# Optimization experiments

Hardware: AMD Instinct MI355X
Metric: run time of the kernel (lower is better)

The kernel has to match this reference:

```python
import jax, jax.numpy as jnp
import numpy as np

N_EMB = 1024
N_HEAD = 16
HEAD_SIZE = N_EMB // N_HEAD  # 64
B, T = 4, 4096


def setup_inputs() -> dict:
    key = jax.random.key(0)
    kx, kq, kk, kv = jax.random.split(key, 4)
    x = jax.random.normal(kx, (B, T, N_EMB), dtype=jnp.float32)
    # torch nn.Linear(in=N_EMB, out=HEAD_SIZE, bias=False) weight: [out, in]
    s = 1.0 / np.sqrt(N_EMB)
    Wq = jax.random.uniform(kq, (HEAD_SIZE, N_EMB), jnp.float32, -s, s)
    Wk = jax.random.uniform(kk, (HEAD_SIZE, N_EMB), jnp.float32, -s, s)
    Wv = jax.random.uniform(kv, (HEAD_SIZE, N_EMB), jnp.float32, -s, s)
    return {"x": x, "Wq": Wq, "Wk": Wk, "Wv": Wv}


def reference(x, Wq, Wk, Wv):
    # q,k,v: [B,T,H]
    q = jnp.einsum('btc,hc->bth', x, Wq)
    k = jnp.einsum('btc,hc->bth', x, Wk)
    v = jnp.einsum('btc,hc->bth', x, Wv)
    scale = HEAD_SIZE ** (-0.5)
    att = jnp.einsum('bth,bsh->bts', q, k) * scale  # [B,T,T]
    Tn = x.shape[1]
    causal = jnp.tril(jnp.ones((Tn, Tn), dtype=bool))
    att = jnp.where(causal, att, -jnp.inf)
    att = jax.nn.softmax(att, axis=-1)
    # dropout p=0.0 -> identity
    out = jnp.einsum('bts,bsh->bth', att, v)  # [B,T,H]
    return out
```

## Files before the change

### kernel.cpp

```cpp
#include <hip/hip_runtime.h>


typedef __attribute__((ext_vector_type(8))) short v8s;
typedef __attribute__((ext_vector_type(4))) float v4f;

static __device__ __forceinline__ unsigned short f2bf(float x) {
  unsigned int u = __builtin_bit_cast(unsigned int, x);
  u += 0x7fffu + ((u >> 16) & 1u);
  return (unsigned short)(u >> 16);
}

__global__ __launch_bounds__(256) void pack_w(const float* __restrict__ Wq,
                                              const float* __restrict__ Wk,
                                              const float* __restrict__ Wv,
                                              unsigned short* __restrict__ WF) {
  int idx = (blockIdx.x * 256 + threadIdx.x) * 4;
  int row = idx >> 10;
  int k   = idx & 1023;
  const float* src;
  float scale;
  if (row < 64)       { src = Wq + row * 1024 + k;         scale = 0.125f; }
  else if (row < 128) { src = Wk + (row - 64) * 1024 + k;  scale = 1.0f;   }
  else                { src = Wv + (row - 128) * 1024 + k; scale = 1.0f;   }
  float4 f = *(const float4*)src;
  ushort4 o;
  o.x = f2bf(f.x * scale); o.y = f2bf(f.y * scale);
  o.z = f2bf(f.z * scale); o.w = f2bf(f.w * scale);
  size_t off = ((size_t)((k >> 8) * 8 + ((k >> 5) & 7)) * 12 + (row >> 4)) * 512 +
               (((k >> 3) & 3) * 16 + (row & 15)) * 8 + (k & 7);
  *(ushort4*)(WF + off) = o;
}

__global__ __launch_bounds__(256, 2) void qkv(const float* __restrict__ x,
                                              const unsigned short* __restrict__ WF,
                                              unsigned short* __restrict__ Qg,
                                              unsigned short* __restrict__ KF,
                                              unsigned short* __restrict__ VF) {
  __shared__ float red[3][64][49];
  const int tid   = threadIdx.x;
  const int lane  = tid & 63;
  const int wv    = tid >> 6;
  const int quad  = lane >> 4;
  const int colid = lane & 15;
  const int row0  = blockIdx.x * 32;

  const float* xbase = x + (size_t)(row0 + colid) * 1024 + wv * 256 + quad * 8;
  const unsigned short* wfbase = WF + (size_t)wv * 8 * 12 * 512 + lane * 8;

  v4f acc[24];
#pragma unroll
  for (int i = 0; i < 24; i++) acc[i] = (v4f){0.f, 0.f, 0.f, 0.f};

#pragma unroll
  for (int step = 0; step < 8; step++) {
    v8s am[2];
#pragma unroll
    for (int mg = 0; mg < 2; mg++) {
      float4 f0 = *(const float4*)(xbase + (size_t)mg * 16 * 1024 + step * 32);
      float4 f1 = *(const float4*)(xbase + (size_t)mg * 16 * 1024 + step * 32 + 4);
      am[mg][0] = (short)f2bf(f0.x); am[mg][1] = (short)f2bf(f0.y);
      am[mg][2] = (short)f2bf(f0.z); am[mg][3] = (short)f2bf(f0.w);
      am[mg][4] = (short)f2bf(f1.x); am[mg][5] = (short)f2bf(f1.y);
      am[mg][6] = (short)f2bf(f1.z); am[mg][7] = (short)f2bf(f1.w);
    }
    v8s bt[12];
#pragma unroll
    for (int nt = 0; nt < 12; nt++)
      bt[nt] = *(const v8s*)(wfbase + (size_t)(step * 12 + nt) * 512);
#pragma unroll
    for (int nt = 0; nt < 12; nt++)
#pragma unroll
      for (int mg = 0; mg < 2; mg++)
        acc[mg * 12 + nt] =
            __builtin_amdgcn_mfma_f32_16x16x32_bf16(am[mg], bt[nt], acc[mg * 12 + nt], 0, 0, 0);
  }

#pragma unroll
  for (int mg = 0; mg < 2; mg++) {
    if (wv != 0) {
#pragma unroll
      for (int nt = 0; nt < 12; nt++)
#pragma unroll
        for (int r = 0; r < 4; r++)
          red[wv - 1][lane][nt * 4 + r] = acc[mg * 12 + nt][r];
    }
    __syncthreads();
    if (wv == 0) {
      const int trow_base = row0 + mg * 16 + quad * 4;
#pragma unroll
      for (int nt = 0; nt < 12; nt++) {
        float sum[4];
#pragma unroll
        for (int r = 0; r < 4; r++)
          sum[r] = acc[mg * 12 + nt][r] + red[0][lane][nt * 4 + r] +
                   red[1][lane][nt * 4 + r] + red[2][lane][nt * 4 + r];
        if (nt < 4) {
#pragma unroll
          for (int r = 0; r < 4; r++)
            Qg[(size_t)(trow_base + r) * 64 + nt * 16 + colid] = f2bf(sum[r]);
        } else if (nt < 8) {
          int half = (nt - 4) >> 1;
          int q_f  = ((nt - 4) * 2 + (colid >> 3)) & 3;
          int j    = colid & 7;
#pragma unroll
          for (int r = 0; r < 4; r++) {
            int t  = trow_base + r;
            int b  = t >> 12, tl = t & 4095;
            int si = tl >> 6, sl = tl & 63;
            KF[((size_t)(b * 64 + si) * 8 + (sl >> 4) * 2 + half) * 512 +
               (q_f * 16 + (sl & 15)) * 8 + j] = f2bf(sum[r]);
          }
        } else {
#pragma unroll
          for (int r = 0; r < 4; r++) {
            int t  = trow_base + r;
            int b  = t >> 12, tl = t & 4095;
            int si = tl >> 6;
            int half = (tl >> 5) & 1, q_f = (tl >> 3) & 3, j = tl & 7;
            VF[((size_t)(b * 64 + si) * 8 + (nt - 8) * 2 + half) * 512 +
               (q_f * 16 + colid) * 8 + j] = f2bf(sum[r]);
          }
        }
      }
    }
    __syncthreads();
  }
}

__global__ __launch_bounds__(256, 2) void flash(const unsigned short* __restrict__ Qg,
                                                const unsigned short* __restrict__ KF,
                                                const unsigned short* __restrict__ VF,
                                                float* __restrict__ out) {
  __shared__ alignas(16) char smem[4 * 32 * 68 * 4 + 4 * 32 * 4];
  unsigned short* pl = (unsigned short*)smem;
  float* redf = (float*)smem;
  float* lred = (float*)(smem + 4 * 32 * 68 * 4);

  const int tid   = threadIdx.x;
  const int lane  = tid & 63;
  const int wv    = tid >> 6;
  const int quad  = lane >> 4;
  const int colid = lane & 15;
  const int qt32  = 127 - (int)(blockIdx.x >> 2);
  const int b     = blockIdx.x & 3;
  const int bT    = b * 4096;
  const int row00 = qt32 * 32;
  const int qimax = (row00 + 31) >> 6;

  v8s qf[2][2];
#pragma unroll
  for (int mt = 0; mt < 2; mt++) {
    const unsigned short* qrow =
        Qg + (size_t)(bT + row00 + mt * 16 + colid) * 64 + quad * 8;
    qf[mt][0] = *(const v8s*)(qrow);
    qf[mt][1] = *(const v8s*)(qrow + 32);
  }

  v8s ones;
#pragma unroll
  for (int j = 0; j < 8; j++) ones[j] = (short)0x3F80;

  v4f o[2][4];
#pragma unroll
  for (int mt = 0; mt < 2; mt++)
#pragma unroll
    for (int i = 0; i < 4; i++) o[mt][i] = (v4f){0.f, 0.f, 0.f, 0.f};
  v4f lac[2];
  lac[0] = (v4f){0.f, 0.f, 0.f, 0.f};
  lac[1] = (v4f){0.f, 0.f, 0.f, 0.f};

  const unsigned short* kb0 = KF + (size_t)b * 64 * 4096 + lane * 8;
  const unsigned short* vb0 = VF + (size_t)b * 64 * 4096 + lane * 8;

  for (int si = wv; si <= qimax; si += 4) {
    const unsigned short* ktile = kb0 + (size_t)si * 4096;
    const unsigned short* vtile = vb0 + (size_t)si * 4096;
    v8s kbr[8], vfr[8];
#pragma unroll
    for (int c = 0; c < 8; c++) kbr[c] = *(const v8s*)(ktile + (size_t)c * 512);
#pragma unroll
    for (int c = 0; c < 8; c++) vfr[c] = *(const v8s*)(vtile + (size_t)c * 512);

#pragma unroll
    for (int mt = 0; mt < 2; mt++) {
      v4f s[4];
#pragma unroll
      for (int i = 0; i < 4; i++) s[i] = (v4f){0.f, 0.f, 0.f, 0.f};
#pragma unroll
      for (int nt = 0; nt < 4; nt++) {
        s[nt] = __builtin_amdgcn_mfma_f32_16x16x32_bf16(qf[mt][0], kbr[2 * nt], s[nt], 0, 0, 0);
        s[nt] = __builtin_amdgcn_mfma_f32_16x16x32_bf16(qf[mt][1], kbr[2 * nt + 1], s[nt], 0, 0, 0);
      }

      if (si == qimax) {
        int rowb = row00 + mt * 16 + quad * 4;
        int colb = si * 64;
#pragma unroll
        for (int nt = 0; nt < 4; nt++)
#pragma unroll
          for (int r = 0; r < 4; r++)
            if (colb + nt * 16 + colid > rowb + r) s[nt][r] = -1e30f;
      }

      unsigned short* pw = pl + (wv * 2 + mt) * (16 * 72);
#pragma unroll
      for (int nt = 0; nt < 4; nt++)
#pragma unroll
        for (int r = 0; r < 4; r++)
          pw[(quad * 4 + r) * 72 + nt * 16 + colid] = f2bf(__expf(s[nt][r]));
    }

#pragma unroll
    for (int mt = 0; mt < 2; mt++) {
      unsigned short* pw = pl + (wv * 2 + mt) * (16 * 72);
#pragma unroll
      for (int ks = 0; ks < 64; ks += 32) {
        v8s af = *(const v8s*)(&pw[colid * 72 + ks + quad * 8]);
        lac[mt] = __builtin_amdgcn_mfma_f32_16x16x32_bf16(af, ones, lac[mt], 0, 0, 0);
#pragma unroll
        for (int nt = 0; nt < 4; nt++)
          o[mt][nt] = __builtin_amdgcn_mfma_f32_16x16x32_bf16(
              af, vfr[2 * nt + (ks >> 5)], o[mt][nt], 0, 0, 0);
      }
    }
  }

  __syncthreads();
#pragma unroll
  for (int mt = 0; mt < 2; mt++) {
#pragma unroll
    for (int nt = 0; nt < 4; nt++)
#pragma unroll
      for (int r = 0; r < 4; r++)
        redf[(wv * 32 + mt * 16 + quad * 4 + r) * 68 + nt * 16 + colid] = o[mt][nt][r];
    if (colid == 0) {
#pragma unroll
      for (int r = 0; r < 4; r++)
        lred[wv * 32 + mt * 16 + quad * 4 + r] = lac[mt][r];
    }
  }
  __syncthreads();

  {
    int col = tid & 63;
    int r0  = tid >> 6;
#pragma unroll
    for (int rr = 0; rr < 8; rr++) {
      int row = r0 * 8 + rr;
      float sum = 0.f, lsum = 0.f;
#pragma unroll
      for (int w = 0; w < 4; w++) {
        sum  += redf[(w * 32 + row) * 68 + col];
        lsum += lred[w * 32 + row];
      }
      out[(size_t)(bT + row00 + row) * 64 + col] = sum / lsum;
    }
  }
}

extern "C" void kernel_launch(void* const* d_in, const int* in_sizes, int n_in,
                              void* d_out, int out_size, void* d_ws, size_t ws_size,
                              hipStream_t stream) {
  const float* x  = (const float*)d_in[0];
  const float* Wq = (const float*)d_in[1];
  const float* Wk = (const float*)d_in[2];
  const float* Wv = (const float*)d_in[3];
  float* out = (float*)d_out;

  unsigned short* WF = (unsigned short*)d_ws;
  unsigned short* Qg = WF + 192 * 1024;
  unsigned short* KF = Qg + 16384 * 64;
  unsigned short* VF = KF + 16384 * 64;

  hipLaunchKernelGGL(pack_w, dim3(192), dim3(256), 0, stream, Wq, Wk, Wv, WF);
  hipLaunchKernelGGL(qkv, dim3(512), dim3(256), 0, stream, x, WF, Qg, KF, VF);
  hipLaunchKernelGGL(flash, dim3(512), dim3(256), 0, stream, Qg, KF, VF, out);
}
```

Measured before the change: 146.4 us.

## Restructure QKV projection with double-buffered LDS DMA staging and no split-K reduction

The QKV projection kernel now uses 128-thread blocks. Each wave owns 16 rows across the full K dimension, so the cross-wave split-K reduction through shared memory is gone. x and packed weight tiles are streamed into double-buffered LDS with global_load_lds DMA, which overlaps loads with MFMA work. The weight packing layout is simplified to a linear K-major order to match the new staging. The cost is about 64KB of LDS per block and a serial 16-step K loop per wave, which may limit occupancy.

```diff
diff --git a/kernel.cpp b/kernel.cpp
--- a/kernel.cpp
+++ b/kernel.cpp
@@ -8,6 +8,12 @@
   unsigned int u = __builtin_bit_cast(unsigned int, x);
   u += 0x7fffu + ((u >> 16) & 1u);
   return (unsigned short)(u >> 16);
+}
+
+static __device__ __forceinline__ void dma16(const void* src, void* dst) {
+  __builtin_amdgcn_global_load_lds(
+      (const __attribute__((address_space(1))) void*)src,
+      (__attribute__((address_space(3))) void*)dst, 16, 0, 0);
 }
 
 __global__ __launch_bounds__(256) void pack_w(const float* __restrict__ Wq,
@@ -26,17 +32,18 @@
   ushort4 o;
   o.x = f2bf(f.x * scale); o.y = f2bf(f.y * scale);
   o.z = f2bf(f.z * scale); o.w = f2bf(f.w * scale);
-  size_t off = ((size_t)((k >> 8) * 8 + ((k >> 5) & 7)) * 12 + (row >> 4)) * 512 +
+  size_t off = ((size_t)(k >> 5) * 12 + (row >> 4)) * 512 +
                (((k >> 3) & 3) * 16 + (row & 15)) * 8 + (k & 7);
   *(ushort4*)(WF + off) = o;
 }
 
-__global__ __launch_bounds__(256, 2) void qkv(const float* __restrict__ x,
-                                              const unsigned short* __restrict__ WF,
-                                              unsigned short* __restrict__ Qg,
-                                              unsigned short* __restrict__ KF,
-                                              unsigned short* __restrict__ VF) {
-  __shared__ float red[3][64][49];
+__global__ __launch_bounds__(128) void qkv(const float* __restrict__ x,
+                                           const unsigned short* __restrict__ WF,
+                                           unsigned short* __restrict__ Qg,
+                                           unsigned short* __restrict__ KF,
+                                           unsigned short* __restrict__ VF) {
+  __shared__ alignas(16) char xs[2][8192];
+  __shared__ alignas(16) char ws[2][24576];
   const int tid   = threadIdx.x;
   const int lane  = tid & 63;
   const int wv    = tid >> 6;
@@ -44,86 +51,84 @@
   const int colid = lane & 15;
   const int row0  = blockIdx.x * 32;
 
-  const float* xbase = x + (size_t)(row0 + colid) * 1024 + wv * 256 + quad * 8;
-  const unsigned short* wfbase = WF + (size_t)wv * 8 * 12 * 512 + lane * 8;
-
-  v4f acc[24];
-#pragma unroll
-  for (int i = 0; i < 24; i++) acc[i] = (v4f){0.f, 0.f, 0.f, 0.f};
-
-#pragma unroll
-  for (int step = 0; step < 8; step++) {
-    v8s am[2];
-#pragma unroll
-    for (int mg = 0; mg < 2; mg++) {
-      float4 f0 = *(const float4*)(xbase + (size_t)mg * 16 * 1024 + step * 32);
-      float4 f1 = *(const float4*)(xbase + (size_t)mg * 16 * 1024 + step * 32 + 4);
-      am[mg][0] = (short)f2bf(f0.x); am[mg][1] = (short)f2bf(f0.y);
-      am[mg][2] = (short)f2bf(f0.z); am[mg][3] = (short)f2bf(f0.w);
-      am[mg][4] = (short)f2bf(f1.x); am[mg][5] = (short)f2bf(f1.y);
-      am[mg][6] = (short)f2bf(f1.z); am[mg][7] = (short)f2bf(f1.w);
-    }
-    v8s bt[12];
-#pragma unroll
-    for (int nt = 0; nt < 12; nt++)
-      bt[nt] = *(const v8s*)(wfbase + (size_t)(step * 12 + nt) * 512);
-#pragma unroll
-    for (int nt = 0; nt < 12; nt++)
-#pragma unroll
-      for (int mg = 0; mg < 2; mg++)
-        acc[mg * 12 + nt] =
-            __builtin_amdgcn_mfma_f32_16x16x32_bf16(am[mg], bt[nt], acc[mg * 12 + nt], 0, 0, 0);
-  }
-
-#pragma unroll
-  for (int mg = 0; mg < 2; mg++) {
-    if (wv != 0) {
-#pragma unroll
-      for (int nt = 0; nt < 12; nt++)
-#pragma unroll
-        for (int r = 0; r < 4; r++)
-          red[wv - 1][lane][nt * 4 + r] = acc[mg * 12 + nt][r];
-    }
+  const char* xB = (const char*)x;
+  const char* WB = (const char*)WF;
+
+  v4f acc[12];
+#pragma unroll
+  for (int i = 0; i < 12; i++) acc[i] = (v4f){0.f, 0.f, 0.f, 0.f};
+
+  auto stage = [&](int kt, int slot) {
+#pragma unroll
+    for (int i = 0; i < 4; i++) {
+      int c   = wv * 4 + i;
+      int cwv = c >> 2, s = (c >> 1) & 1, h = c & 1;
+      const char* src = xB + (size_t)(row0 + cwv * 16 + colid) * 4096 +
+                        kt * 256 + s * 128 + quad * 32 + h * 16;
+      dma16(src, &xs[slot][c * 1024]);
+    }
+#pragma unroll
+    for (int i = 0; i < 12; i++) {
+      int id = wv * 12 + i;
+      int s = id / 12, nt = id % 12;
+      const char* src = WB + ((size_t)(kt * 2 + s) * 12 + nt) * 1024 + lane * 16;
+      dma16(src, &ws[slot][id * 1024]);
+    }
+  };
+
+  stage(0, 0);
+
+  for (int kt = 0; kt < 16; kt++) {
+    const int slot = kt & 1;
     __syncthreads();
-    if (wv == 0) {
-      const int trow_base = row0 + mg * 16 + quad * 4;
+    if (kt < 15) stage(kt + 1, slot ^ 1);
+#pragma unroll
+    for (int s = 0; s < 2; s++) {
+      float4 f0 = *(const float4*)(&xs[slot][(wv * 4 + s * 2 + 0) * 1024 + lane * 16]);
+      float4 f1 = *(const float4*)(&xs[slot][(wv * 4 + s * 2 + 1) * 1024 + lane * 16]);
+      v8s a;
+      a[0] = (short)f2bf(f0.x); a[1] = (short)f2bf(f0.y);
+      a[2] = (short)f2bf(f0.z); a[3] = (short)f2bf(f0.w);
+      a[4] = (short)f2bf(f1.x); a[5] = (short)f2bf(f1.y);
+      a[6] = (short)f2bf(f1.z); a[7] = (short)f2bf(f1.w);
 #pragma unroll
       for (int nt = 0; nt < 12; nt++) {
-        float sum[4];
-#pragma unroll
-        for (int r = 0; r < 4; r++)
-          sum[r] = acc[mg * 12 + nt][r] + red[0][lane][nt * 4 + r] +
-                   red[1][lane][nt * 4 + r] + red[2][lane][nt * 4 + r];
-        if (nt < 4) {
-#pragma unroll
-          for (int r = 0; r < 4; r++)
-            Qg[(size_t)(trow_base + r) * 64 + nt * 16 + colid] = f2bf(sum[r]);
-        } else if (nt < 8) {
-          int half = (nt - 4) >> 1;
-          int q_f  = ((nt - 4) * 2 + (colid >> 3)) & 3;
-          int j    = colid & 7;
-#pragma unroll
-          for (int r = 0; r < 4; r++) {
-            int t  = trow_base + r;
-            int b  = t >> 12, tl = t & 4095;
-            int si = tl >> 6, sl = tl & 63;
-            KF[((size_t)(b * 64 + si) * 8 + (sl >> 4) * 2 + half) * 512 +
-               (q_f * 16 + (sl & 15)) * 8 + j] = f2bf(sum[r]);
-          }
-        } else {
-#pragma unroll
-          for (int r = 0; r < 4; r++) {
-            int t  = trow_base + r;
-            int b  = t >> 12, tl = t & 4095;
-            int si = tl >> 6;
-            int half = (tl >> 5) & 1, q_f = (tl >> 3) & 3, j = tl & 7;
-            VF[((size_t)(b * 64 + si) * 8 + (nt - 8) * 2 + half) * 512 +
-               (q_f * 16 + colid) * 8 + j] = f2bf(sum[r]);
-          }
-        }
-      }
-    }
-    __syncthreads();
+        v8s b = *(const v8s*)(&ws[slot][(s * 12 + nt) * 1024 + lane * 16]);
+        acc[nt] = __builtin_amdgcn_mfma_f32_16x16x32_bf16(a, b, acc[nt], 0, 0, 0);
+      }
+    }
+  }
+
+  const int trow_base = row0 + wv * 16 + quad * 4;
+#pragma unroll
+  for (int nt = 0; nt < 12; nt++) {
+    if (nt < 4) {
+#pragma unroll
+      for (int r = 0; r < 4; r++)
+        Qg[(size_t)(trow_base + r) * 64 + nt * 16 + colid] = f2bf(acc[nt][r]);
+    } else if (nt < 8) {
+      int half = (nt - 4) >> 1;
+      int q_f  = ((nt - 4) * 2 + (colid >> 3)) & 3;
+      int j    = colid & 7;
+#pragma unroll
+      for (int r = 0; r < 4; r++) {
+        int t  = trow_base + r;
+        int b  = t >> 12, tl = t & 4095;
+        int si = tl >> 6, sl = tl & 63;
+        KF[((size_t)(b * 64 + si) * 8 + (sl >> 4) * 2 + half) * 512 +
+           (q_f * 16 + (sl & 15)) * 8 + j] = f2bf(acc[nt][r]);
+      }
+    } else {
+#pragma unroll
+      for (int r = 0; r < 4; r++) {
+        int t  = trow_base + r;
+        int b  = t >> 12, tl = t & 4095;
+        int si = tl >> 6;
+        int half = (tl >> 5) & 1, q_f = (tl >> 3) & 3, j = tl & 7;
+        VF[((size_t)(b * 64 + si) * 8 + (nt - 8) * 2 + half) * 512 +
+           (q_f * 16 + colid) * 8 + j] = f2bf(acc[nt][r]);
+      }
+    }
   }
 }
 
@@ -175,11 +180,11 @@
   for (int si = wv; si <= qimax; si += 4) {
     const unsigned short* ktile = kb0 + (size_t)si * 4096;
     const unsigned short* vtile = vb0 + (size_t)si * 4096;
-    v8s kbr[8], vfr[8];
-#pragma unroll
-    for (int c = 0; c < 8; c++) kbr[c] = *(const v8s*)(ktile + (size_t)c * 512);
-#pragma unroll
-    for (int c = 0; c < 8; c++) vfr[c] = *(const v8s*)(vtile + (size_t)c * 512);
+    v8s ck[8], cv[8];
+#pragma unroll
+    for (int c = 0; c < 8; c++) ck[c] = *(const v8s*)(ktile + (size_t)c * 512);
+#pragma unroll
+    for (int c = 0; c < 8; c++) cv[c] = *(const v8s*)(vtile + (size_t)c * 512);
 
 #pragma unroll
     for (int mt = 0; mt < 2; mt++) {
@@ -188,8 +193,8 @@
       for (int i = 0; i < 4; i++) s[i] = (v4f){0.f, 0.f, 0.f, 0.f};
 #pragma unroll
       for (int nt = 0; nt < 4; nt++) {
-        s[nt] = __builtin_amdgcn_mfma_f32_16x16x32_bf16(qf[mt][0], kbr[2 * nt], s[nt], 0, 0, 0);
-        s[nt] = __builtin_amdgcn_mfma_f32_16x16x32_bf16(qf[mt][1], kbr[2 * nt + 1], s[nt], 0, 0, 0);
+        s[nt] = __builtin_amdgcn_mfma_f32_16x16x32_bf16(qf[mt][0], ck[2 * nt], s[nt], 0, 0, 0);
+        s[nt] = __builtin_amdgcn_mfma_f32_16x16x32_bf16(qf[mt][1], ck[2 * nt + 1], s[nt], 0, 0, 0);
       }
 
       if (si == qimax) {
@@ -220,7 +225,7 @@
 #pragma unroll
         for (int nt = 0; nt < 4; nt++)
           o[mt][nt] = __builtin_amdgcn_mfma_f32_16x16x32_bf16(
-              af, vfr[2 * nt + (ks >> 5)], o[mt][nt], 0, 0, 0);
+              af, cv[2 * nt + (ks >> 5)], o[mt][nt], 0, 0, 0);
       }
     }
   }
@@ -273,6 +278,6 @@
   unsigned short* VF = KF + 16384 * 64;
 
   hipLaunchKernelGGL(pack_w, dim3(192), dim3(256), 0, stream, Wq, Wk, Wv, WF);
-  hipLaunchKernelGGL(qkv, dim3(512), dim3(256), 0, stream, x, WF, Qg, KF, VF);
+  hipLaunchKernelGGL(qkv, dim3(512), dim3(128), 0, stream, x, WF, Qg, KF, VF);
   hipLaunchKernelGGL(flash, dim3(512), dim3(256), 0, stream, Qg, KF, VF, out);
 }
```

After: 143.0 us. 1.02x faster.
